# Kernel tuning notes

Hardware: AMD Instinct MI355X
Metric: run time of the kernel (lower is better)

Reference implementation:

```python
import jax, jax.numpy as jnp
import numpy as np

MEAN = jnp.array([0.485, 0.456, 0.406], dtype=jnp.float32).reshape(3, 1, 1)
STD = jnp.array([0.229, 0.224, 0.225], dtype=jnp.float32).reshape(3, 1, 1)
BLOCK = 8  # JPEG DCT block size


def _conv2(x, k):
    # x: [B,H,W], k: [kh,kw] -> SAME conv per image
    kern = k[None, None].astype(x.dtype)
    y = jax.lax.conv_general_dilated(x[:, None], kern, (1, 1), 'SAME')
    return y[:, 0]


def _box3(x):
    return _conv2(x, jnp.ones((3, 3), jnp.float32) / 9.0)


def _normalize(f):
    # per-image min-max to [0,1]; zero map if degenerate (matches _normalize)
    fmin = f.min(axis=(-2, -1), keepdims=True)
    fmax = f.max(axis=(-2, -1), keepdims=True)
    rng = fmax - fmin
    safe = jnp.where(rng < 1e-8, 1.0, rng)
    return jnp.where(rng < 1e-8, 0.0, (f - fmin) / safe)


def _forward(x):
    # denormalize ImageNet stats, clamp, scale to [0,255] (continuous; uint8 round omitted)
    img = jnp.clip(x * STD + MEAN, 0.0, 1.0) * 255.0  # [B,3,H,W]
    gray = 0.299 * img[:, 0] + 0.587 * img[:, 1] + 0.114 * img[:, 2]  # [B,H,W]

    # --- channel 0: spectral residual anomaly (FFT) ---
    F = jnp.fft.fft2(gray)
    logmag = jnp.log(jnp.abs(F) + 1e-8)
    resid = logmag - _box3(logmag)            # high-freq log-spectrum residual
    phase = jnp.angle(F)
    sal = jnp.abs(jnp.fft.ifft2(jnp.exp(resid) * jnp.exp(1j * phase))) ** 2
    M_spec = _normalize(sal)

    # --- channel 1: resampling artifact (2nd-derivative / Laplacian magnitude) ---
    lap_k = jnp.array([[0., 1., 0.], [1., -4., 1.], [0., 1., 0.]], jnp.float32)
    M_resamp = _normalize(jnp.abs(_conv2(gray, lap_k)))

    # --- channel 2: JPEG blockiness (gradient energy on 8x8 block boundaries) ---
    B, H, W = gray.shape
    dh = jnp.abs(gray - jnp.roll(gray, 1, axis=-1))  # horizontal neighbor diff
    dv = jnp.abs(gray - jnp.roll(gray, 1, axis=-2))  # vertical neighbor diff
    col_mask = (jnp.arange(W) % BLOCK == 0).astype(gray.dtype)  # [W]
    row_mask = (jnp.arange(H) % BLOCK == 0).astype(gray.dtype)  # [H]
    blockiness = dh * col_mask[None, None, :] + dv * row_mask[None, :, None]
    M_jpeg = _normalize(blockiness)

    return jnp.stack([M_spec, M_resamp, M_jpeg], axis=1)  # [B,3,H,W]


def setup_inputs() -> dict:
    key = jax.random.key(0)
    x = jax.random.normal(key, (16, 3, 512, 512), dtype=jnp.float32)
    return {"x": x}


def reference(x):
    return _forward(x)
```

## Files before the change

### kernel.cpp

```cpp
#include <hip/hip_runtime.h>
#include <hip/hip_bf16.h>
#include <math.h>

#define W 512
#define H 512
#define HW 262144
#define NB 16

__device__ __forceinline__ int brev9(int x) { return (int)(__brev((unsigned)x) >> 23); }

__device__ __forceinline__ void block_minmax_atomic(float vmin, float vmax,
                                                    unsigned* minU, unsigned* maxU) {
  #pragma unroll
  for (int o = 32; o; o >>= 1) {
    vmin = fminf(vmin, __shfl_xor(vmin, o));
    vmax = fmaxf(vmax, __shfl_xor(vmax, o));
  }
  __shared__ float smin[4], smax[4];
  int wid = threadIdx.x >> 6;
  int lane = threadIdx.x & 63;
  if (lane == 0) { smin[wid] = vmin; smax[wid] = vmax; }
  __syncthreads();
  if (threadIdx.x == 0) {
    float m = smin[0], M = smax[0];
    #pragma unroll
    for (int i = 1; i < 4; ++i) { m = fminf(m, smin[i]); M = fmaxf(M, smax[i]); }
    atomicMin(minU, __float_as_uint(m));
    atomicMax(maxU, __float_as_uint(M));
  }
  __syncthreads();
}

__global__ void k_init(unsigned* mm) {
  int t = threadIdx.x;
  if (t < 48) mm[t] = 0x7F800000u;
  else if (t < 96) mm[t] = 0u;
}

__device__ __forceinline__ float gray_one(float r, float g, float b) {
  float R = fminf(fmaxf(fmaf(r, 0.229f, 0.485f), 0.f), 1.f) * 255.f;
  float G = fminf(fmaxf(fmaf(g, 0.224f, 0.456f), 0.f), 1.f) * 255.f;
  float B = fminf(fmaxf(fmaf(b, 0.225f, 0.406f), 0.f), 1.f) * 255.f;
  return fmaf(0.299f, R, fmaf(0.587f, G, 0.114f * B));
}

__global__ void k_gray(const float* __restrict__ x, float* __restrict__ gray) {
  int i4 = blockIdx.x * blockDim.x + threadIdx.x;
  int pix = i4 << 2;
  int b = pix >> 18;
  int hw = pix & (HW - 1);
  const float4 r4 = *(const float4*)(x + (((size_t)(b * 3 + 0)) << 18) + hw);
  const float4 g4 = *(const float4*)(x + (((size_t)(b * 3 + 1)) << 18) + hw);
  const float4 b4 = *(const float4*)(x + (((size_t)(b * 3 + 2)) << 18) + hw);
  float4 o;
  o.x = gray_one(r4.x, g4.x, b4.x);
  o.y = gray_one(r4.y, g4.y, b4.y);
  o.z = gray_one(r4.z, g4.z, b4.z);
  o.w = gray_one(r4.w, g4.w, b4.w);
  *(float4*)(gray + (((size_t)b) << 18) + hw) = o;
}

__global__ void k_ch12(const float* __restrict__ gray, float* __restrict__ out, unsigned* mm) {
  int slab = blockIdx.x, b = blockIdx.y, t = threadIdx.x;
  const float* gb = gray + (((size_t)b) << 18);
  float* o1 = out + (((size_t)(b * 3 + 1)) << 18);
  float* o2 = out + (((size_t)(b * 3 + 2)) << 18);
  float mn1 = INFINITY, mx1 = -INFINITY, mn2 = INFINITY, mx2 = -INFINITY;
  for (int i4 = t; i4 < 32 * 128; i4 += 256) {
    int r = (slab << 5) + (i4 >> 7);
    int k4 = (i4 & 127) << 2;
    const float* row = gb + r * W;
    float4 c4 = *(const float4*)(row + k4);
    float s_lfw = row[(k4 + W - 1) & (W - 1)];
    float s_rt  = (k4 < W - 4) ? row[k4 + 4] : 0.f;
    float4 up4 = (r > 0)     ? *(const float4*)(gb + (r - 1) * W + k4) : make_float4(0.f, 0.f, 0.f, 0.f);
    float4 dn4 = (r < H - 1) ? *(const float4*)(gb + (r + 1) * W + k4) : make_float4(0.f, 0.f, 0.f, 0.f);
    float c[4]  = {c4.x, c4.y, c4.z, c4.w};
    float up[4] = {up4.x, up4.y, up4.z, up4.w};
    float dn[4] = {dn4.x, dn4.y, dn4.z, dn4.w};
    float lap[4], blk[4];
    #pragma unroll
    for (int e = 0; e < 4; ++e) {
      float lf = (e == 0) ? ((k4 > 0) ? s_lfw : 0.f) : c[e - 1];
      float rt = (e == 3) ? s_rt : c[e + 1];
      lap[e] = fabsf(lf + rt + up[e] + dn[e] - 4.f * c[e]);
      mn1 = fminf(mn1, lap[e]); mx1 = fmaxf(mx1, lap[e]);
    }
    bool rowb = ((r & 7) == 0);
    float pv[4] = {0.f, 0.f, 0.f, 0.f};
    if (rowb) {
      int rp = (r + H - 1) & (H - 1);
      float4 p4 = *(const float4*)(gb + rp * W + k4);
      pv[0] = p4.x; pv[1] = p4.y; pv[2] = p4.z; pv[3] = p4.w;
    }
    #pragma unroll
    for (int e = 0; e < 4; ++e) {
      float v = 0.f;
      if (e == 0 && ((k4 & 7) == 0)) v += fabsf(c[0] - s_lfw);
      if (rowb) v += fabsf(c[e] - pv[e]);
      blk[e] = v;
      mn2 = fminf(mn2, v); mx2 = fmaxf(mx2, v);
    }
    *(float4*)(o1 + r * W + k4) = make_float4(lap[0], lap[1], lap[2], lap[3]);
    *(float4*)(o2 + r * W + k4) = make_float4(blk[0], blk[1], blk[2], blk[3]);
  }
  block_minmax_atomic(mn1, mx1, mm + (b * 3 + 1), mm + 48 + (b * 3 + 1));
  block_minmax_atomic(mn2, mx2, mm + (b * 3 + 2), mm + 48 + (b * 3 + 2));
}

template <int DIR>
__device__ __forceinline__ void fft512(float* sre, float* sim, int t) {
  #pragma unroll
  for (int s = 1; s <= 9; ++s) {
    int half = 1 << (s - 1);
    __syncthreads();
    int j = t & (half - 1);
    int i0 = ((t >> (s - 1)) << s) + j;
    int i1 = i0 + half;
    float ang = (float)DIR * -6.283185307179586f * (float)j / (float)(1 << s);
    float sn, cs;
    __sincosf(ang, &sn, &cs);
    float ur = sre[i0], ui = sim[i0];
    float vr = sre[i1], vi = sim[i1];
    float tr = fmaf(vr, cs, -vi * sn);
    float ti = fmaf(vr, sn, vi * cs);
    sre[i0] = ur + tr; sim[i0] = ui + ti;
    sre[i1] = ur - tr; sim[i1] = ui - ti;
  }
  __syncthreads();
}

template <int DIR>
__device__ __forceinline__ void fft512x8(float* sre, float* sim, int c, int tc) {
  #pragma unroll
  for (int s = 1; s <= 9; ++s) {
    int half = 1 << (s - 1);
    __syncthreads();
    #pragma unroll
    for (int bb = 0; bb < 8; ++bb) {
      int bf = tc + (bb << 5);
      int j = bf & (half - 1);
      int i0 = ((bf >> (s - 1)) << s) + j;
      int i1 = i0 + half;
      float ang = (float)DIR * -6.283185307179586f * (float)j / (float)(1 << s);
      float sn, cs;
      __sincosf(ang, &sn, &cs);
      int a0 = i0 * 9 + c, a1 = i1 * 9 + c;
      float ur = sre[a0], ui = sim[a0];
      float vr = sre[a1], vi = sim[a1];
      float tr = fmaf(vr, cs, -vi * sn);
      float ti = fmaf(vr, sn, vi * cs);
      sre[a0] = ur + tr; sim[a0] = ui + ti;
      sre[a1] = ur - tr; sim[a1] = ui - ti;
    }
  }
  __syncthreads();
}

__global__ void k_rowfft(const float* __restrict__ gray, float2* __restrict__ C) {
  int r = blockIdx.x, b = blockIdx.y, t = threadIdx.x;
  __shared__ float sre[512], sim[512];
  const float* g = gray + (((size_t)b) << 18) + r * W;
  #pragma unroll
  for (int k = t; k < 512; k += 256) {
    int kr = brev9(k);
    sre[kr] = g[k]; sim[kr] = 0.f;
  }
  fft512<1>(sre, sim, t);
  float2* Crow = C + (((size_t)b) << 18) + r * W;
  #pragma unroll
  for (int k = t; k < 512; k += 256) Crow[k] = make_float2(sre[k], sim[k]);
}

__global__ void k_colfft_fwd(float2* __restrict__ C, float* __restrict__ L) {
  int b = blockIdx.y, col0 = blockIdx.x << 3, t = threadIdx.x;
  __shared__ float sre[512 * 9], sim[512 * 9];
  float2* Cb = C + (((size_t)b) << 18);
  int c = t & 7, q = t >> 3;
  #pragma unroll
  for (int it = 0; it < 16; ++it) {
    int r = (it << 5) + q;
    float2 v = Cb[r * W + col0 + c];
    int rr = brev9(r);
    sre[rr * 9 + c] = v.x; sim[rr * 9 + c] = v.y;
  }
  fft512x8<1>(sre, sim, t >> 5, t & 31);
  float* Lb = L + (((size_t)b) << 18);
  #pragma unroll
  for (int it = 0; it < 16; ++it) {
    int r = (it << 5) + q;
    float re = sre[r * 9 + c], im = sim[r * 9 + c];
    Cb[r * W + col0 + c] = make_float2(re, im);
    Lb[r * W + col0 + c] = logf(sqrtf(fmaf(re, re, im * im)) + 1e-8f);
  }
}

__global__ void k_rowifft_g(float2* __restrict__ C, const float* __restrict__ L) {
  int r = blockIdx.x, b = blockIdx.y, t = threadIdx.x;
  __shared__ float sre[512], sim[512], l0[512], lm[512], lp[512];
  const float* Lb = L + (((size_t)b) << 18);
  #pragma unroll
  for (int k = t; k < 512; k += 256) {
    l0[k] = Lb[r * W + k];
    lm[k] = (r > 0) ? Lb[(r - 1) * W + k] : 0.f;
    lp[k] = (r < H - 1) ? Lb[(r + 1) * W + k] : 0.f;
  }
  __syncthreads();
  float2* Crow = C + (((size_t)b) << 18) + r * W;
  #pragma unroll
  for (int k = t; k < 512; k += 256) {
    float sum = lm[k] + l0[k] + lp[k];
    if (k > 0)     sum += lm[k - 1] + l0[k - 1] + lp[k - 1];
    if (k < W - 1) sum += lm[k + 1] + l0[k + 1] + lp[k + 1];
    float resid = l0[k] - sum * (1.f / 9.f);
    float2 cv = Crow[k];
    float mag = sqrtf(fmaf(cv.x, cv.x, cv.y * cv.y));
    float er = __expf(resid);
    float gr, gi;
    if (mag > 1e-30f) { float tt = er / mag; gr = cv.x * tt; gi = cv.y * tt; }
    else { gr = er; gi = 0.f; }
    int kr = brev9(k);
    sre[kr] = gr; sim[kr] = gi;
  }
  fft512<-1>(sre, sim, t);
  #pragma unroll
  for (int k = t; k < 512; k += 256)
    Crow[k] = make_float2(sre[k] * (1.f / 512.f), sim[k] * (1.f / 512.f));
}

__global__ void k_colifft_sal(const float2* __restrict__ C, float* __restrict__ out, unsigned* mm) {
  int b = blockIdx.y, col0 = blockIdx.x << 3, t = threadIdx.x;
  __shared__ float sre[512 * 9], sim[512 * 9];
  const float2* Cb = C + (((size_t)b) << 18);
  int c = t & 7, q = t >> 3;
  #pragma unroll
  for (int it = 0; it < 16; ++it) {
    int r = (it << 5) + q;
    float2 v = Cb[r * W + col0 + c];
    int rr = brev9(r);
    sre[rr * 9 + c] = v.x; sim[rr * 9 + c] = v.y;
  }
  fft512x8<-1>(sre, sim, t >> 5, t & 31);
  float* ob = out + (((size_t)(b * 3 + 0)) << 18);
  float mn = INFINITY, mx = -INFINITY;
  #pragma unroll
  for (int it = 0; it < 16; ++it) {
    int r = (it << 5) + q;
    float re = sre[r * 9 + c], im = sim[r * 9 + c];
    float sal = fmaf(re, re, im * im) * 3.814697265625e-6f;
    ob[r * W + col0 + c] = sal;
    mn = fminf(mn, sal); mx = fmaxf(mx, sal);
  }
  block_minmax_atomic(mn, mx, mm + b * 3, mm + 48 + b * 3);
}

__global__ void k_norm(float* __restrict__ out, const unsigned* __restrict__ mm) {
  int i = blockIdx.x * blockDim.x + threadIdx.x;
  size_t base = ((size_t)i) << 2;
  int map = (int)(base >> 18);
  float mn = __uint_as_float(mm[map]);
  float mx = __uint_as_float(mm[48 + map]);
  float rng = mx - mn;
  float4 v = *(float4*)(out + base);
  float4 o;
  if (rng < 1e-8f) {
    o = make_float4(0.f, 0.f, 0.f, 0.f);
  } else {
    float inv = 1.f / rng;
    o.x = (v.x - mn) * inv;
    o.y = (v.y - mn) * inv;
    o.z = (v.z - mn) * inv;
    o.w = (v.w - mn) * inv;
  }
  *(float4*)(out + base) = o;
}

extern "C" void kernel_launch(void* const* d_in, const int* in_sizes, int n_in,
                              void* d_out, int out_size, void* d_ws, size_t ws_size,
                              hipStream_t stream) {
  const float* x = (const float*)d_in[0];
  float* out = (float*)d_out;

  float* gray = (float*)d_ws;
  float2* C = (float2*)((char*)d_ws + (size_t)NB * HW * sizeof(float));
  float* L = (float*)((char*)C + (size_t)NB * HW * sizeof(float2));
  unsigned* mm = (unsigned*)((char*)L + (size_t)NB * HW * sizeof(float));

  k_init<<<1, 96, 0, stream>>>(mm);
  k_gray<<<4096, 256, 0, stream>>>(x, gray);
  k_ch12<<<dim3(16, NB), 256, 0, stream>>>(gray, out, mm);
  k_rowfft<<<dim3(H, NB), 256, 0, stream>>>(gray, C);
  k_colfft_fwd<<<dim3(W / 8, NB), 256, 0, stream>>>(C, L);
  k_rowifft_g<<<dim3(H, NB), 256, 0, stream>>>(C, L);
  k_colifft_sal<<<dim3(W / 8, NB), 256, 0, stream>>>(C, out, mm);
  k_norm<<<12288, 256, 0, stream>>>(out, mm);
}
```

Measured before the change: 241.1 us.

## Fuse grayscale conversion into row FFT and use shared-memory twiddle tables

Removes the separate grayscale kernel: the row-FFT kernel now reads the RGB input, computes gray, writes it for the channel 1/2 kernel, and transforms it in place. This drops one kernel launch and one extra read of the gray buffer. All four FFT kernels now precompute a 256-entry twiddle table in shared memory instead of calling sincos in every butterfly, swapping transcendental math for shared-memory loads. The twiddle table takes a little more LDS per block, and the strided table reads may hit bank conflicts.

Result: faster. 233.5 us (-3.2%).

```diff
diff --git a/kernel.cpp b/kernel.cpp
--- a/kernel.cpp
+++ b/kernel.cpp
@@ -44,20 +44,85 @@
   return fmaf(0.299f, R, fmaf(0.587f, G, 0.114f * B));
 }
 
-__global__ void k_gray(const float* __restrict__ x, float* __restrict__ gray) {
-  int i4 = blockIdx.x * blockDim.x + threadIdx.x;
-  int pix = i4 << 2;
-  int b = pix >> 18;
-  int hw = pix & (HW - 1);
-  const float4 r4 = *(const float4*)(x + (((size_t)(b * 3 + 0)) << 18) + hw);
-  const float4 g4 = *(const float4*)(x + (((size_t)(b * 3 + 1)) << 18) + hw);
-  const float4 b4 = *(const float4*)(x + (((size_t)(b * 3 + 2)) << 18) + hw);
-  float4 o;
-  o.x = gray_one(r4.x, g4.x, b4.x);
-  o.y = gray_one(r4.y, g4.y, b4.y);
-  o.z = gray_one(r4.z, g4.z, b4.z);
-  o.w = gray_one(r4.w, g4.w, b4.w);
-  *(float4*)(gray + (((size_t)b) << 18) + hw) = o;
+__device__ __forceinline__ void tw_init(float2* tw, int t) {
+  if (t < 256) {
+    float sn, cs;
+    __sincosf(-6.283185307179586f * (float)t * (1.f / 512.f), &sn, &cs);
+    tw[t] = make_float2(cs, sn);
+  }
+}
+
+template <int DIR>
+__device__ __forceinline__ void fft512_tw(float* sre, float* sim, const float2* tw, int t) {
+  #pragma unroll
+  for (int s = 1; s <= 9; ++s) {
+    __syncthreads();
+    int half = 1 << (s - 1);
+    int j = t & (half - 1);
+    int i0 = ((t >> (s - 1)) << s) + j;
+    int i1 = i0 + half;
+    float2 w = tw[j << (9 - s)];
+    float cs = w.x;
+    float sn = (DIR > 0) ? w.y : -w.y;
+    float ur = sre[i0], ui = sim[i0];
+    float vr = sre[i1], vi = sim[i1];
+    float tr = fmaf(vr, cs, -vi * sn);
+    float ti = fmaf(vr, sn, vi * cs);
+    sre[i0] = ur + tr; sim[i0] = ui + ti;
+    sre[i1] = ur - tr; sim[i1] = ui - ti;
+  }
+  __syncthreads();
+}
+
+template <int DIR>
+__device__ __forceinline__ void fft512x8_tw(float* sre, float* sim, const float2* tw,
+                                            int c, int tc) {
+  #pragma unroll
+  for (int s = 1; s <= 9; ++s) {
+    __syncthreads();
+    int half = 1 << (s - 1);
+    #pragma unroll
+    for (int bb = 0; bb < 8; ++bb) {
+      int bf = tc + (bb << 5);
+      int j = bf & (half - 1);
+      int i0 = ((bf >> (s - 1)) << s) + j;
+      int i1 = i0 + half;
+      float2 w = tw[j << (9 - s)];
+      float cs = w.x;
+      float sn = (DIR > 0) ? w.y : -w.y;
+      int a0 = i0 * 9 + c, a1 = i1 * 9 + c;
+      float ur = sre[a0], ui = sim[a0];
+      float vr = sre[a1], vi = sim[a1];
+      float tr = fmaf(vr, cs, -vi * sn);
+      float ti = fmaf(vr, sn, vi * cs);
+      sre[a0] = ur + tr; sim[a0] = ui + ti;
+      sre[a1] = ur - tr; sim[a1] = ui - ti;
+    }
+  }
+  __syncthreads();
+}
+
+__global__ void k_rowfft(const float* __restrict__ x, float* __restrict__ gray,
+                         float2* __restrict__ C) {
+  int r = blockIdx.x, b = blockIdx.y, t = threadIdx.x;
+  __shared__ float sre[512], sim[512];
+  __shared__ float2 tw[256];
+  tw_init(tw, t);
+  const float* xr = x + (((size_t)(b * 3 + 0)) << 18) + r * W;
+  const float* xg = x + (((size_t)(b * 3 + 1)) << 18) + r * W;
+  const float* xb = x + (((size_t)(b * 3 + 2)) << 18) + r * W;
+  float* gr = gray + (((size_t)b) << 18) + r * W;
+  #pragma unroll
+  for (int k = t; k < 512; k += 256) {
+    float g = gray_one(xr[k], xg[k], xb[k]);
+    gr[k] = g;
+    int kr = brev9(k);
+    sre[kr] = g; sim[kr] = 0.f;
+  }
+  fft512_tw<1>(sre, sim, tw, t);
+  float2* Crow = C + (((size_t)b) << 18) + r * W;
+  #pragma unroll
+  for (int k = t; k < 512; k += 256) Crow[k] = make_float2(sre[k], sim[k]);
 }
 
 __global__ void k_ch12(const float* __restrict__ gray, float* __restrict__ out, unsigned* mm) {
@@ -108,73 +173,11 @@
   block_minmax_atomic(mn2, mx2, mm + (b * 3 + 2), mm + 48 + (b * 3 + 2));
 }
 
-template <int DIR>
-__device__ __forceinline__ void fft512(float* sre, float* sim, int t) {
-  #pragma unroll
-  for (int s = 1; s <= 9; ++s) {
-    int half = 1 << (s - 1);
-    __syncthreads();
-    int j = t & (half - 1);
-    int i0 = ((t >> (s - 1)) << s) + j;
-    int i1 = i0 + half;
-    float ang = (float)DIR * -6.283185307179586f * (float)j / (float)(1 << s);
-    float sn, cs;
-    __sincosf(ang, &sn, &cs);
-    float ur = sre[i0], ui = sim[i0];
-    float vr = sre[i1], vi = sim[i1];
-    float tr = fmaf(vr, cs, -vi * sn);
-    float ti = fmaf(vr, sn, vi * cs);
-    sre[i0] = ur + tr; sim[i0] = ui + ti;
-    sre[i1] = ur - tr; sim[i1] = ui - ti;
-  }
-  __syncthreads();
-}
-
-template <int DIR>
-__device__ __forceinline__ void fft512x8(float* sre, float* sim, int c, int tc) {
-  #pragma unroll
-  for (int s = 1; s <= 9; ++s) {
-    int half = 1 << (s - 1);
-    __syncthreads();
-    #pragma unroll
-    for (int bb = 0; bb < 8; ++bb) {
-      int bf = tc + (bb << 5);
-      int j = bf & (half - 1);
-      int i0 = ((bf >> (s - 1)) << s) + j;
-      int i1 = i0 + half;
-      float ang = (float)DIR * -6.283185307179586f * (float)j / (float)(1 << s);
-      float sn, cs;
-      __sincosf(ang, &sn, &cs);
-      int a0 = i0 * 9 + c, a1 = i1 * 9 + c;
-      float ur = sre[a0], ui = sim[a0];
-      float vr = sre[a1], vi = sim[a1];
-      float tr = fmaf(vr, cs, -vi * sn);
-      float ti = fmaf(vr, sn, vi * cs);
-      sre[a0] = ur + tr; sim[a0] = ui + ti;
-      sre[a1] = ur - tr; sim[a1] = ui - ti;
-    }
-  }
-  __syncthreads();
-}
-
-__global__ void k_rowfft(const float* __restrict__ gray, float2* __restrict__ C) {
-  int r = blockIdx.x, b = blockIdx.y, t = threadIdx.x;
-  __shared__ float sre[512], sim[512];
-  const float* g = gray + (((size_t)b) << 18) + r * W;
-  #pragma unroll
-  for (int k = t; k < 512; k += 256) {
-    int kr = brev9(k);
-    sre[kr] = g[k]; sim[kr] = 0.f;
-  }
-  fft512<1>(sre, sim, t);
-  float2* Crow = C + (((size_t)b) << 18) + r * W;
-  #pragma unroll
-  for (int k = t; k < 512; k += 256) Crow[k] = make_float2(sre[k], sim[k]);
-}
-
 __global__ void k_colfft_fwd(float2* __restrict__ C, float* __restrict__ L) {
   int b = blockIdx.y, col0 = blockIdx.x << 3, t = threadIdx.x;
   __shared__ float sre[512 * 9], sim[512 * 9];
+  __shared__ float2 tw[256];
+  tw_init(tw, t);
   float2* Cb = C + (((size_t)b) << 18);
   int c = t & 7, q = t >> 3;
   #pragma unroll
@@ -184,7 +187,7 @@
     int rr = brev9(r);
     sre[rr * 9 + c] = v.x; sim[rr * 9 + c] = v.y;
   }
-  fft512x8<1>(sre, sim, t >> 5, t & 31);
+  fft512x8_tw<1>(sre, sim, tw, t >> 5, t & 31);
   float* Lb = L + (((size_t)b) << 18);
   #pragma unroll
   for (int it = 0; it < 16; ++it) {
@@ -198,6 +201,8 @@
 __global__ void k_rowifft_g(float2* __restrict__ C, const float* __restrict__ L) {
   int r = blockIdx.x, b = blockIdx.y, t = threadIdx.x;
   __shared__ float sre[512], sim[512], l0[512], lm[512], lp[512];
+  __shared__ float2 tw[256];
+  tw_init(tw, t);
   const float* Lb = L + (((size_t)b) << 18);
   #pragma unroll
   for (int k = t; k < 512; k += 256) {
@@ -222,7 +227,7 @@
     int kr = brev9(k);
     sre[kr] = gr; sim[kr] = gi;
   }
-  fft512<-1>(sre, sim, t);
+  fft512_tw<-1>(sre, sim, tw, t);
   #pragma unroll
   for (int k = t; k < 512; k += 256)
     Crow[k] = make_float2(sre[k] * (1.f / 512.f), sim[k] * (1.f / 512.f));
@@ -231,6 +236,8 @@
 __global__ void k_colifft_sal(const float2* __restrict__ C, float* __restrict__ out, unsigned* mm) {
   int b = blockIdx.y, col0 = blockIdx.x << 3, t = threadIdx.x;
   __shared__ float sre[512 * 9], sim[512 * 9];
+  __shared__ float2 tw[256];
+  tw_init(tw, t);
   const float2* Cb = C + (((size_t)b) << 18);
   int c = t & 7, q = t >> 3;
   #pragma unroll
@@ -240,7 +247,7 @@
     int rr = brev9(r);
     sre[rr * 9 + c] = v.x; sim[rr * 9 + c] = v.y;
   }
-  fft512x8<-1>(sre, sim, t >> 5, t & 31);
+  fft512x8_tw<-1>(sre, sim, tw, t >> 5, t & 31);
   float* ob = out + (((size_t)(b * 3 + 0)) << 18);
   float mn = INFINITY, mx = -INFINITY;
   #pragma unroll
@@ -287,9 +294,8 @@
   unsigned* mm = (unsigned*)((char*)L + (size_t)NB * HW * sizeof(float));
 
   k_init<<<1, 96, 0, stream>>>(mm);
-  k_gray<<<4096, 256, 0, stream>>>(x, gray);
+  k_rowfft<<<dim3(H, NB), 256, 0, stream>>>(x, gray, C);
   k_ch12<<<dim3(16, NB), 256, 0, stream>>>(gray, out, mm);
-  k_rowfft<<<dim3(H, NB), 256, 0, stream>>>(gray, C);
   k_colfft_fwd<<<dim3(W / 8, NB), 256, 0, stream>>>(C, L);
   k_rowifft_g<<<dim3(H, NB), 256, 0, stream>>>(C, L);
   k_colifft_sal<<<dim3(W / 8, NB), 256, 0, stream>>>(C, out, mm);
```
